# Performance work log

Measured on AMD Instinct MI355X. Metric: run time of the kernel, lower is better.

## Reference

```python
import jax, jax.numpy as jnp
import numpy as np

B, S, D = 1, 2048, 3072
H, DH = 24, 128
ENC, NIP = 512, 64
COND = (512 // 8) * (512 // 8) * 16 // 64  # 1024 cond tokens per lora
RANK, ALPHA, LW, IP_SCALE = 16, 16.0, 1.0, 1.0
EPS = 1e-5


def _rms(x):
    return x * jax.lax.rsqrt(jnp.mean(x * x, axis=-1, keepdims=True) + EPS)


def _to_heads(x):
    b, s, _ = x.shape
    return x.reshape(b, s, H, DH).transpose(0, 2, 1, 3)  # [B,H,S,DH]


def _from_heads(x):
    b, h, s, d = x.shape
    return x.transpose(0, 2, 1, 3).reshape(b, s, h * d)


def _lora(x, dn, up):
    # token mask keeps only the cond block (number=0, n_loras=1 -> last COND tokens)
    y = ((x[:, -COND:, :] @ dn) @ up) * (ALPHA / RANK)
    z = jnp.zeros((x.shape[0], x.shape[1] - COND, up.shape[1]), x.dtype)
    return jnp.concatenate([z, y], axis=1)


def _sdpa(q, k, v, mask=None):
    s = jnp.einsum('bhqd,bhkd->bhqk', q, k) * (1.0 / np.sqrt(DH))
    if mask is not None:
        s = s + mask
    return jnp.einsum('bhqk,bhkd->bhqd', jax.nn.softmax(s, axis=-1), v)


def _forward(hidden_states, encoder_hidden_states, image_emb,
             Wq, bq, Wk, bk, Wv, bv, Waq, baq, Wak, bak, Wav, bav,
             Wo, bo, Wao, bao, Wkip, Wvip,
             lq_dn, lq_up, lk_dn, lk_up, lv_dn, lv_up, lp_dn, lp_up):
    hs, ehs, img = hidden_states, encoder_hidden_states, image_emb
    # context (encoder) projections + RMSNorm on q/k
    eq = _rms(_to_heads(ehs @ Waq + baq))
    ek = _rms(_to_heads(ehs @ Wak + bak))
    ev = _to_heads(ehs @ Wav + bav)
    # main-stream q/k/v with masked LoRA branches
    q = hs @ Wq + bq + LW * _lora(hs, lq_dn, lq_up)
    k = hs @ Wk + bk + LW * _lora(hs, lk_dn, lk_up)
    v = hs @ Wv + bv + LW * _lora(hs, lv_dn, lv_up)
    q = _rms(_to_heads(q))
    k = _rms(_to_heads(k))
    v = _to_heads(v)
    # IP-adapter branch: extra K/V from image_emb, norm_added_k is RMSNorm(128)
    kip = _rms(_to_heads(img @ Wkip))
    vip = _to_heads(img @ Wvip)
    ip_out = _from_heads(_sdpa(q, kip, vip))  # [B,S,D]
    # concat encoder stream ahead of main stream
    q = jnp.concatenate([eq, q], axis=2)
    k = jnp.concatenate([ek, k], axis=2)
    v = jnp.concatenate([ev, v], axis=2)
    SL = ENC + S
    SB = SL - COND  # scaled_block_size
    m = jnp.ones((SL, SL), jnp.float32)
    m = m.at[:SB, :].set(0.0)        # non-cond rows attend everywhere
    m = m.at[SB:, SB:].set(0.0)      # single cond block attends to itself (n_loras=1)
    mask = m * (-1e20)
    out = _from_heads(_sdpa(q, k, v, mask))  # [B,SL,D]
    enc_out = out[:, :ENC, :]
    main = out[:, ENC:, :] + IP_SCALE * ip_out
    main = main @ Wo + bo
    main = main + LW * _lora(main, lp_dn, lp_up)  # proj LoRA (to_out dropout=identity)
    enc_out = enc_out @ Wao + bao
    return jnp.concatenate([enc_out, main], axis=1)  # [B, ENC+S, D]


def setup_inputs():
    key = jax.random.key(0)
    ks = iter(jax.random.split(key, 40))
    w = lambda *sh: jax.random.normal(next(ks), sh, jnp.float32) * 0.02
    return dict(
        hidden_states=jax.random.normal(next(ks), (B, S, D), jnp.float32),
        encoder_hidden_states=jax.random.normal(next(ks), (B, ENC, D), jnp.float32),
        image_emb=jax.random.normal(next(ks), (B, NIP, D), jnp.float32),
        Wq=w(D, D), bq=w(D), Wk=w(D, D), bk=w(D), Wv=w(D, D), bv=w(D),
        Waq=w(D, D), baq=w(D), Wak=w(D, D), bak=w(D), Wav=w(D, D), bav=w(D),
        Wo=w(D, D), bo=w(D), Wao=w(D, D), bao=w(D),
        Wkip=w(D, D), Wvip=w(D, D),
        lq_dn=w(D, RANK), lq_up=w(RANK, D), lk_dn=w(D, RANK), lk_up=w(RANK, D),
        lv_dn=w(D, RANK), lv_up=w(RANK, D), lp_dn=w(D, RANK), lp_up=w(RANK, D),
    )


def reference(hidden_states, encoder_hidden_states, image_emb,
              Wq, bq, Wk, bk, Wv, bv, Waq, baq, Wak, bak, Wav, bav,
              Wo, bo, Wao, bao, Wkip, Wvip,
              lq_dn, lq_up, lk_dn, lk_up, lv_dn, lv_up, lp_dn, lp_up):
    return _forward(hidden_states, encoder_hidden_states, image_emb,
                    Wq, bq, Wk, bk, Wv, bv, Waq, baq, Wak, bak, Wav, bav,
                    Wo, bo, Wao, bao, Wkip, Wvip,
                    lq_dn, lq_up, lk_dn, lk_up, lv_dn, lv_up, lp_dn, lp_up)
```

## Files before the change

kernel.cpp:

```cpp
#include <hip/hip_runtime.h>

typedef unsigned short u16;
typedef short s16x8 __attribute__((ext_vector_type(8)));
typedef float f32x4 __attribute__((ext_vector_type(4)));
typedef const __attribute__((address_space(1))) unsigned int* as1_u32p;
typedef __attribute__((address_space(3))) unsigned int* as3_u32p;

static_assert(sizeof(s16x8) == 16, "");

struct alignas(8) U16x4 { u16 x, y, z, w; };

__device__ __forceinline__ u16 f2bf(float f) {
  union { float f; unsigned u; } c; c.f = f;
  return (u16)((c.u + 0x7fffu + ((c.u >> 16) & 1u)) >> 16);
}
__device__ __forceinline__ float bf2f(u16 h) {
  union { unsigned u; float f; } c; c.u = ((unsigned)h) << 16;
  return c.f;
}
__device__ __forceinline__ void async16(const void* g, void* l) {
  __builtin_amdgcn_global_load_lds((as1_u32p)g, (as3_u32p)l, 16, 0, 0);
}

__launch_bounds__(256)
__global__ void cvt_bf16(const float* __restrict__ in, u16* __restrict__ out, long n) {
  long i = ((long)blockIdx.x * 256 + threadIdx.x) * 8;
  if (i >= n) return;
  float4 a = *(const float4*)(in + i);
  float4 b = *(const float4*)(in + i + 4);
  U16x4 o0{f2bf(a.x), f2bf(a.y), f2bf(a.z), f2bf(a.w)};
  U16x4 o1{f2bf(b.x), f2bf(b.y), f2bf(b.z), f2bf(b.w)};
  *(U16x4*)(out + i) = o0;
  *(U16x4*)(out + i + 4) = o1;
}

__launch_bounds__(256)
__global__ void cvt_hs(const float* __restrict__ hs, const float* __restrict__ tl,
                       u16* __restrict__ hsb) {
  long idx = (long)blockIdx.x * 256 + threadIdx.x;
  long m = idx / 392, c = idx % 392;
  U16x4 o0, o1;
  if (c < 384) {
    const float* p = hs + m * 3072 + c * 8;
    float4 a = *(const float4*)p;
    float4 b = *(const float4*)(p + 4);
    o0 = U16x4{f2bf(a.x), f2bf(a.y), f2bf(a.z), f2bf(a.w)};
    o1 = U16x4{f2bf(b.x), f2bf(b.y), f2bf(b.z), f2bf(b.w)};
  } else {
    u16 t[8];
#pragma unroll
    for (int i = 0; i < 8; ++i) {
      int r = (int)(c - 384) * 8 + i;
      float v = (m >= 1024 && r < 48) ? tl[(m - 1024) * 48 + r] : 0.f;
      t[i] = f2bf(v);
    }
    o0 = U16x4{t[0], t[1], t[2], t[3]};
    o1 = U16x4{t[4], t[5], t[6], t[7]};
  }
  u16* d = hsb + m * 3136 + c * 8;
  *(U16x4*)d = o0;
  *(U16x4*)(d + 4) = o1;
}

__launch_bounds__(256)
__global__ void pack_bias(const float* __restrict__ a, const float* __restrict__ b,
                          const float* __restrict__ c, float* __restrict__ out) {
  int i = blockIdx.x * 256 + threadIdx.x;
  if (i >= 9216) return;
  out[i] = (i < 3072) ? a[i] : (i < 6144) ? b[i - 3072] : c[i - 6144];
}

struct WTArgs { const float* src[3]; u16* dst[3]; };

__launch_bounds__(256)
__global__ void transpose_w(WTArgs args, int ldd) {
  const float* src = args.src[blockIdx.z];
  u16* dst = args.dst[blockIdx.z];
  __shared__ float tile[32][33];
  int k0 = blockIdx.x * 32, n0 = blockIdx.y * 32;
  int r = threadIdx.x >> 3, c4 = (threadIdx.x & 7) * 4;
  float4 v = *(const float4*)(src + (long)(k0 + r) * 3072 + n0 + c4);
  tile[r][c4 + 0] = v.x; tile[r][c4 + 1] = v.y;
  tile[r][c4 + 2] = v.z; tile[r][c4 + 3] = v.w;
  __syncthreads();
  U16x4 o{f2bf(tile[c4 + 0][r]), f2bf(tile[c4 + 1][r]),
          f2bf(tile[c4 + 2][r]), f2bf(tile[c4 + 3][r])};
  *(U16x4*)(dst + (long)(n0 + r) * ldd + k0 + c4) = o;
}

__launch_bounds__(256)
__global__ void fill_wtail(const float* __restrict__ u0, const float* __restrict__ u1,
                           const float* __restrict__ u2, u16* __restrict__ WTb) {
  int idx = blockIdx.x * 256 + threadIdx.x;
  int n = idx >> 6, i = idx & 63;
  int seg = n / 3072;
  const float* up = (seg == 0) ? u0 : (seg == 1) ? u1 : u2;
  int r = i - seg * 16;
  float v = (r >= 0 && r < 16) ? up[(long)r * 3072 + (n - seg * 3072)] : 0.f;
  WTb[(long)n * 3136 + 3072 + i] = f2bf(v);
}

__launch_bounds__(256)
__global__ void transpose_v(const u16* __restrict__ VB, u16* __restrict__ VT, int T) {
  __shared__ u16 tile[32][34];
  int h = blockIdx.z;
  int t0 = blockIdx.x * 32, d0 = blockIdx.y * 32;
  int r = threadIdx.x >> 3, c4 = (threadIdx.x & 7) * 4;
  U16x4 v = *(const U16x4*)(VB + ((long)h * T + t0 + r) * 128 + d0 + c4);
  tile[r][c4 + 0] = v.x; tile[r][c4 + 1] = v.y;
  tile[r][c4 + 2] = v.z; tile[r][c4 + 3] = v.w;
  __syncthreads();
  U16x4 o{tile[c4 + 0][r], tile[c4 + 1][r], tile[c4 + 2][r], tile[c4 + 3][r]};
  *(U16x4*)(VT + ((long)h * 128 + d0 + r) * T + t0 + c4) = o;
}

__launch_bounds__(256)
__global__ void rms_heads4(const float* __restrict__ in, int col0,
                           u16* __restrict__ out, int do_rms) {
  const int t = blockIdx.x;
  const int w = threadIdx.x >> 6, lane = threadIdx.x & 63;
  const long ps = 64LL * 6144;
#pragma unroll
  for (int hh = 0; hh < 6; ++hh) {
    int h = w * 6 + hh;
    const float* x = in + (long)t * 6144 + col0 + h * 128 + lane * 2;
    float a = x[0] + x[ps] + x[2 * ps] + x[3 * ps];
    float b = x[1] + x[1 + ps] + x[1 + 2 * ps] + x[1 + 3 * ps];
    float scale = 1.f;
    if (do_rms) {
      float ss = a * a + b * b;
#pragma unroll
      for (int st = 1; st < 64; st <<= 1) ss += __shfl_xor(ss, st, 64);
      scale = rsqrtf(ss * (1.f / 128.f) + 1e-5f);
    }
    unsigned pa = f2bf(a * scale), pb = f2bf(b * scale);
    *(unsigned*)(out + ((long)h * 64 + t) * 128 + lane * 2) = pa | (pb << 16);
  }
}

__launch_bounds__(256)
__global__ void lora_dn3(const float* __restrict__ X, int ldx,
                         const float* __restrict__ d0, const float* __restrict__ d1,
                         const float* __restrict__ d2, float* __restrict__ t) {
  __shared__ float red[4][48];
  const int m = blockIdx.x;
  const float* xr = X + (long)m * ldx;
  float p[48];
#pragma unroll
  for (int r = 0; r < 48; ++r) p[r] = 0.f;
  for (int k = threadIdx.x; k < 3072; k += 256) {
    float a = xr[k];
    const float* e0 = d0 + (long)k * 16;
    const float* e1 = d1 + (long)k * 16;
    const float* e2 = d2 + (long)k * 16;
#pragma unroll
    for (int r = 0; r < 16; ++r) {
      p[r]      += a * e0[r];
      p[16 + r] += a * e1[r];
      p[32 + r] += a * e2[r];
    }
  }
#pragma unroll
  for (int r = 0; r < 48; ++r)
#pragma unroll
    for (int st = 1; st < 64; st <<= 1) p[r] += __shfl_xor(p[r], st, 64);
  int lane = threadIdx.x & 63, w = threadIdx.x >> 6;
  if (lane == 0) {
#pragma unroll
    for (int r = 0; r < 48; ++r) red[w][r] = p[r];
  }
  __syncthreads();
  if (threadIdx.x < 48) {
    int r = threadIdx.x;
    t[(long)m * 48 + r] = red[0][r] + red[1][r] + red[2][r] + red[3][r];
  }
}

__launch_bounds__(256)
__global__ void lora_dn(const float* __restrict__ X, int ldx,
                        const float* __restrict__ dn, float* __restrict__ t) {
  __shared__ float red[4][16];
  const int m = blockIdx.x;
  const float* xr = X + (long)m * ldx;
  float p[16];
#pragma unroll
  for (int r = 0; r < 16; ++r) p[r] = 0.f;
  for (int k = threadIdx.x; k < 3072; k += 256) {
    float a = xr[k];
    const float* d = dn + (long)k * 16;
#pragma unroll
    for (int r = 0; r < 16; ++r) p[r] += a * d[r];
  }
#pragma unroll
  for (int r = 0; r < 16; ++r)
#pragma unroll
    for (int st = 1; st < 64; st <<= 1) p[r] += __shfl_xor(p[r], st, 64);
  int lane = threadIdx.x & 63, w = threadIdx.x >> 6;
  if (lane == 0) {
#pragma unroll
    for (int r = 0; r < 16; ++r) red[w][r] = p[r];
  }
  __syncthreads();
  if (threadIdx.x < 16) {
    int r = threadIdx.x;
    t[(long)m * 16 + r] = red[0][r] + red[1][r] + red[2][r] + red[3][r];
  }
}

__launch_bounds__(256)
__global__ void lora_up(const float* __restrict__ t, const float* __restrict__ up,
                        float* __restrict__ Y, int ldy) {
  const int m = blockIdx.x;
  float tv[16];
#pragma unroll
  for (int r = 0; r < 16; ++r) tv[r] = t[(long)m * 16 + r];
  float* yr = Y + (long)m * ldy;
  for (int n = threadIdx.x; n < 3072; n += 256) {
    float a = 0.f;
#pragma unroll
    for (int r = 0; r < 16; ++r) a += tv[r] * up[(long)r * 3072 + n];
    yr[n] += a;
  }
}

template <int BM, int MI, int NI>
__launch_bounds__(256)
__global__ void gemm_f32(const u16* __restrict__ A, int lda,
                         const u16* __restrict__ B, int ldb,
                         float* __restrict__ C, int ldc,
                         const float* __restrict__ bias, int KC, long cstride) {
  constexpr int WCOLS = 128 / (NI * 16);
  constexpr int ABYTES = BM * 128;
  __shared__ char smem[ABYTES + 128 * 128];
  char* As = smem;
  char* Bs = smem + ABYTES;
  const int tid = threadIdx.x;
  const int w = tid >> 6, lane = tid & 63;
  const int lr = lane & 15, lg = lane >> 4;
  const int wr = w / WCOLS, wc = w % WCOLS;
  const int nbx = gridDim.x;
  const int nwg = nbx * gridDim.y;
  const int flat = blockIdx.y * nbx + blockIdx.x;
  const int swz = (flat & 7) * (nwg >> 3) + (flat >> 3);
  const long m0 = (long)(swz % nbx) * BM;
  const long n0 = (long)(swz / nbx) * 128;
  const int k0 = blockIdx.z * KC;
  C += blockIdx.z * cstride;
  f32x4 acc[MI][NI] = {};
  constexpr int ACH = BM / 32;
  for (int kb = k0; kb < k0 + KC; kb += 64) {
    __syncthreads();
#pragma unroll
    for (int i = 0; i < ACH; ++i) {
      int x = (tid + 256 * i) * 16;
      int row = x >> 7;
      int sx = x ^ ((row & 7) << 4);
      async16((const char*)(A + (m0 + row) * lda + kb) + (sx & 127),
              As + ((w << 10) + (i << 12)));
    }
#pragma unroll
    for (int i = 0; i < 4; ++i) {
      int x = (tid + 256 * i) * 16;
      int row = x >> 7;
      int sx = x ^ ((row & 7) << 4);
      async16((const char*)(B + (n0 + row) * ldb + kb) + (sx & 127),
              Bs + ((w << 10) + (i << 12)));
    }
    __syncthreads();
#pragma unroll
    for (int kc = 0; kc < 2; ++kc) {
      s16x8 af[MI], bfr[NI];
#pragma unroll
      for (int mi = 0; mi < MI; ++mi) {
        int row = wr * (MI * 16) + mi * 16 + lr;
        int b = ((row << 7) + kc * 64 + lg * 16) ^ ((row & 7) << 4);
        af[mi] = *(const s16x8*)(As + b);
      }
#pragma unroll
      for (int ni = 0; ni < NI; ++ni) {
        int row = wc * (NI * 16) + ni * 16 + lr;
        int b = ((row << 7) + kc * 64 + lg * 16) ^ ((row & 7) << 4);
        bfr[ni] = *(const s16x8*)(Bs + b);
      }
#pragma unroll
      for (int mi = 0; mi < MI; ++mi)
#pragma unroll
        for (int ni = 0; ni < NI; ++ni)
          acc[mi][ni] = __builtin_amdgcn_mfma_f32_16x16x32_bf16(af[mi], bfr[ni], acc[mi][ni], 0, 0, 0);
    }
  }
#pragma unroll
  for (int mi = 0; mi < MI; ++mi) {
#pragma unroll
    for (int ni = 0; ni < NI; ++ni) {
      long col = n0 + wc * (NI * 16) + ni * 16 + lr;
      float bv = bias ? bias[col] : 0.f;
#pragma unroll
      for (int j = 0; j < 4; ++j) {
        long row = m0 + wr * (MI * 16) + mi * 16 + lg * 4 + j;
        C[row * ldc + col] = acc[mi][ni][j] + bv;
      }
    }
  }
}

__launch_bounds__(256, 2)
__global__ void gemm_qkv(const u16* __restrict__ A, int lda,
                         const u16* __restrict__ B, int ldb,
                         u16* __restrict__ Qo, u16* __restrict__ Ko, u16* __restrict__ VTo,
                         int t0, const float* __restrict__ bias, int K) {
  __shared__ char smem[49152];
  char* As = smem;
  char* Bs = smem + 16384;
  const int tid = threadIdx.x;
  const int w = tid >> 6, lane = tid & 63;
  const int lr = lane & 15, lg = lane >> 4;
  const int wr = w >> 1, wc = w & 1;
  const int nbx = gridDim.x;
  const int nwg = nbx * gridDim.y;
  const int flat = blockIdx.y * nbx + blockIdx.x;
  const int swz = (flat & 7) * (nwg >> 3) + (flat >> 3);
  const long m0 = (long)(swz % nbx) * 128;
  const long n0 = (long)(swz / nbx) * 256;
  f32x4 acc[4][8] = {};
  for (int kb = 0; kb < K; kb += 64) {
    __syncthreads();
#pragma unroll
    for (int i = 0; i < 4; ++i) {
      int x = (tid + 256 * i) * 16;
      int row = x >> 7;
      int sx = (x & 127) ^ ((row & 7) << 4);
      async16((const char*)(A + (m0 + row) * lda + kb) + sx, As + x);
    }
#pragma unroll
    for (int i = 0; i < 8; ++i) {
      int x = (tid + 256 * i) * 16;
      int row = x >> 7;
      int sx = (x & 127) ^ ((row & 7) << 4);
      async16((const char*)(B + (n0 + row) * ldb + kb) + sx, Bs + x);
    }
    __syncthreads();
#pragma unroll
    for (int kc = 0; kc < 2; ++kc) {
      s16x8 af[4], bfr[8];
#pragma unroll
      for (int mi = 0; mi < 4; ++mi) {
        int row = wr * 64 + mi * 16 + lr;
        af[mi] = *(const s16x8*)(As + (row << 7) + ((kc * 64 + lg * 16) ^ ((row & 7) << 4)));
      }
#pragma unroll
      for (int ni = 0; ni < 8; ++ni) {
        int row = wc * 128 + ni * 16 + lr;
        bfr[ni] = *(const s16x8*)(Bs + (row << 7) + ((kc * 64 + lg * 16) ^ ((row & 7) << 4)));
      }
#pragma unroll
      for (int mi = 0; mi < 4; ++mi)
#pragma unroll
        for (int ni = 0; ni < 8; ++ni)
          acc[mi][ni] = __builtin_amdgcn_mfma_f32_16x16x32_bf16(af[mi], bfr[ni], acc[mi][ni], 0, 0, 0);
    }
  }
  const int seg = (int)(n0 / 3072);
  const int head0 = (int)((n0 % 3072) >> 7);
#pragma unroll
  for (int ni = 0; ni < 8; ++ni) {
    float bv = bias[n0 + wc * 128 + ni * 16 + lr];
#pragma unroll
    for (int mi = 0; mi < 4; ++mi)
#pragma unroll
      for (int j = 0; j < 4; ++j) acc[mi][ni][j] += bv;
  }
  float scl[4][4];
  if (seg < 2) {
#pragma unroll
    for (int mi = 0; mi < 4; ++mi)
#pragma unroll
      for (int j = 0; j < 4; ++j) {
        float s = 0.f;
#pragma unroll
        for (int ni = 0; ni < 8; ++ni) s += acc[mi][ni][j] * acc[mi][ni][j];
#pragma unroll
        for (int st = 1; st < 16; st <<= 1) s += __shfl_xor(s, st, 16);
        scl[mi][j] = rsqrtf(s * (1.f / 128.f) + 1e-5f);
      }
  }
#pragma unroll
  for (int ph = 0; ph < 2; ++ph) {
    __syncthreads();
    if (wc == ph) {
      if (seg < 2) {
#pragma unroll
        for (int mi = 0; mi < 4; ++mi)
#pragma unroll
          for (int ni = 0; ni < 8; ++ni) {
            int d2 = (ni * 16 + lr) * 2;
#pragma unroll
            for (int j = 0; j < 4; ++j) {
              int tok = wr * 64 + mi * 16 + lg * 4 + j;
              *(u16*)(smem + tok * 256 + (d2 ^ ((tok & 7) << 4))) =
                  f2bf(acc[mi][ni][j] * scl[mi][j]);
            }
          }
      } else {
#pragma unroll
        for (int mi = 0; mi < 4; ++mi)
#pragma unroll
          for (int ni = 0; ni < 8; ++ni) {
            int d = ni * 16 + lr;
            int tok0b = (wr * 64 + mi * 16 + lg * 4) * 2;
            U16x4 o{f2bf(acc[mi][ni][0]), f2bf(acc[mi][ni][1]),
                    f2bf(acc[mi][ni][2]), f2bf(acc[mi][ni][3])};
            *(U16x4*)(smem + d * 256 + (tok0b ^ ((d & 7) << 4))) = o;
          }
      }
    }
    __syncthreads();
    const int headp = head0 + ph;
#pragma unroll
    for (int i = 0; i < 8; ++i) {
      int x = (tid + 256 * i) * 16;
      int row = x >> 8, col = x & 255;
      s16x8 vdat = *(const s16x8*)(smem + row * 256 + (col ^ ((row & 7) << 4)));
      if (seg < 2) {
        u16* g = (seg == 0 ? Qo : Ko) + ((long)headp * 2560 + t0 + m0 + row) * 128;
        *(s16x8*)((char*)g + col) = vdat;
      } else {
        u16* g = VTo + ((long)headp * 128 + row) * 2560 + t0 + m0;
        *(s16x8*)((char*)g + col) = vdat;
      }
    }
  }
}

__launch_bounds__(256)
__global__ void gemm_out(const u16* __restrict__ Atok, const u16* __restrict__ WT,
                         float* __restrict__ outp, const float* __restrict__ bao,
                         const float* __restrict__ bo) {
  __shared__ char smem[128 * 128 + 128 * 128];
  char* As = smem;
  char* Bs = smem + 128 * 128;
  const int tid = threadIdx.x;
  const int w = tid >> 6, lane = tid & 63;
  const int lr = lane & 15, lg = lane >> 4;
  const int wr = w >> 1, wc = w & 1;
  const int flat = blockIdx.y * 20 + blockIdx.x;
  const int swz = (flat & 7) * 60 + (flat >> 3);
  const int mx = swz % 20;
  const long n0 = (long)(swz / 20) * 128;
  const u16* A;
  const u16* B;
  const float* bias;
  float* C;
  long m0;
  if (mx < 4) { A = Atok; B = WT; bias = bao; C = outp; m0 = (long)mx * 128; }
  else { A = Atok + 512L * 3072; B = WT + 3072L * 3136; bias = bo; C = outp + 512L * 3072; m0 = (long)(mx - 4) * 128; }
  f32x4 acc[4][4] = {};
  for (int kb = 0; kb < 3072; kb += 64) {
    __syncthreads();
#pragma unroll
    for (int i = 0; i < 4; ++i) {
      int x = (tid + 256 * i) * 16;
      int row = x >> 7;
      int sx = x ^ ((row & 7) << 4);
      async16((const char*)(A + (m0 + row) * 3072 + kb) + (sx & 127),
              As + ((w << 10) + (i << 12)));
    }
#pragma unroll
    for (int i = 0; i < 4; ++i) {
      int x = (tid + 256 * i) * 16;
      int row = x >> 7;
      int sx = x ^ ((row & 7) << 4);
      async16((const char*)(B + (n0 + row) * 3136 + kb) + (sx & 127),
              Bs + ((w << 10) + (i << 12)));
    }
    __syncthreads();
#pragma unroll
    for (int kc = 0; kc < 2; ++kc) {
      s16x8 af[4], bfr[4];
#pragma unroll
      for (int mi = 0; mi < 4; ++mi) {
        int row = wr * 64 + mi * 16 + lr;
        int b = ((row << 7) + kc * 64 + lg * 16) ^ ((row & 7) << 4);
        af[mi] = *(const s16x8*)(As + b);
      }
#pragma unroll
      for (int ni = 0; ni < 4; ++ni) {
        int row = wc * 64 + ni * 16 + lr;
        int b = ((row << 7) + kc * 64 + lg * 16) ^ ((row & 7) << 4);
        bfr[ni] = *(const s16x8*)(Bs + b);
      }
#pragma unroll
      for (int mi = 0; mi < 4; ++mi)
#pragma unroll
        for (int ni = 0; ni < 4; ++ni)
          acc[mi][ni] = __builtin_amdgcn_mfma_f32_16x16x32_bf16(af[mi], bfr[ni], acc[mi][ni], 0, 0, 0);
    }
  }
#pragma unroll
  for (int mi = 0; mi < 4; ++mi) {
#pragma unroll
    for (int ni = 0; ni < 4; ++ni) {
      long col = n0 + wc * 64 + ni * 16 + lr;
      float bv = bias[col];
#pragma unroll
      for (int j = 0; j < 4; ++j) {
        long row = m0 + wr * 64 + mi * 16 + lg * 4 + j;
        C[row * 3072 + col] = acc[mi][ni][j] + bv;
      }
    }
  }
}

__launch_bounds__(512, 4)
__global__ void attn_fused(const u16* __restrict__ QB, const u16* __restrict__ KB,
                           const u16* __restrict__ VT, const u16* __restrict__ KipB,
                           const u16* __restrict__ VipT, u16* __restrict__ OutTok) {
  __shared__ char smem[81920];
  const int tid = threadIdx.x, w = tid >> 6, lane = tid & 63;
  const int lr = lane & 15, lg = lane >> 4;
  const int h = blockIdx.y;
  const int q0 = blockIdx.x * 128;
  const bool ip = (q0 >= 512);
  const u16* Qrow = QB + (long)(h * 2560 + q0 + w * 16 + lr) * 128;
  s16x8 qf[4];
#pragma unroll
  for (int dc = 0; dc < 4; ++dc) qf[dc] = *(const s16x8*)(Qrow + dc * 32 + lg * 8);
  f32x4 accO[8] = {};
  float l_r[4] = {0.f, 0.f, 0.f, 0.f};
  const int kv0 = (q0 >= 1536) ? 1536 : 0;
  const float sc = 0.08838834764831845f;

  auto stage_main = [&](int kv, int buf) {
#pragma unroll
    for (int i = 0; i < 2; ++i) {
      int x = (tid + 512 * i) * 16;
      int row = x >> 8;
      int sx = x ^ ((row & 7) << 4);
      async16((const char*)(KB + (long)(h * 2560 + kv + row) * 128) + (sx & 255),
              smem + buf * 16384 + ((i << 13) + (w << 10)));
    }
#pragma unroll
    for (int i = 0; i < 2; ++i) {
      int x = (tid + 512 * i) * 16;
      int row = x >> 7;
      int sx = x ^ ((row & 7) << 4);
      async16((const char*)(VT + (long)(h * 128 + row) * 2560 + kv) + (sx & 127),
              smem + 32768 + buf * 16384 + ((i << 13) + (w << 10)));
    }
  };
  auto stage_ip = [&](int buf) {
#pragma unroll
    for (int i = 0; i < 2; ++i) {
      int x = (tid + 512 * i) * 16;
      int row = x >> 8;
      int sx = x ^ ((row & 7) << 4);
// ... 43 lines not shown
#pragma unroll
    for (int kc = 0; kc < 2; ++kc) {
      int pb = ((lr << 7) + kc * 64 + lg * 16) ^ ((lr & 7) << 4);
      s16x8 pf = *(const s16x8*)(Pw + pb);
#pragma unroll
      for (int dt = 0; dt < 8; ++dt) {
        int row = dt * 16 + lr;
        int b = ((row << 7) + kc * 64 + lg * 16) ^ ((row & 7) << 4);
        s16x8 vf = *(const s16x8*)(Vs + b);
        accO[dt] = __builtin_amdgcn_mfma_f32_16x16x32_bf16(pf, vf, accO[dt], 0, 0, 0);
      }
    }
    __syncthreads();
    cur ^= 1;
  }
#pragma unroll
  for (int j = 0; j < 4; ++j) {
#pragma unroll
    for (int st = 1; st < 16; st <<= 1) l_r[j] += __shfl_xor(l_r[j], st, 16);
    l_r[j] = 1.f / l_r[j];
  }
#pragma unroll
  for (int dt = 0; dt < 8; ++dt)
#pragma unroll
    for (int j = 0; j < 4; ++j) accO[dt][j] *= l_r[j];
  if (ip) {
    const char* Ks = smem + cur * 16384;
    const char* Vs = smem + 32768 + cur * 16384;
    char* Pw = smem + 65536 + w * 2048;
    f32x4 s2[4] = {};
#pragma unroll
    for (int kt = 0; kt < 4; ++kt)
#pragma unroll
      for (int dc = 0; dc < 4; ++dc) {
        int row = kt * 16 + lr;
        int b = ((row << 8) + dc * 64 + lg * 16) ^ ((row & 7) << 4);
        s16x8 kf = *(const s16x8*)(Ks + b);
        s2[kt] = __builtin_amdgcn_mfma_f32_16x16x32_bf16(qf[dc], kf, s2[kt], 0, 0, 0);
      }
    float p2[4][4];
    float l2[4] = {0.f, 0.f, 0.f, 0.f};
#pragma unroll
    for (int kt = 0; kt < 4; ++kt)
#pragma unroll
      for (int j = 0; j < 4; ++j) {
        float pv = __expf(fmaf(s2[kt][j], sc, -12.0f));
        p2[kt][j] = pv;
        l2[j] += pv;
      }
#pragma unroll
    for (int j = 0; j < 4; ++j) {
#pragma unroll
      for (int st = 1; st < 16; st <<= 1) l2[j] += __shfl_xor(l2[j], st, 16);
      l2[j] = 1.f / l2[j];
    }
#pragma unroll
    for (int kt = 0; kt < 4; ++kt)
#pragma unroll
      for (int j = 0; j < 4; ++j) {
        int prow = lg * 4 + j;
        int b = ((prow << 7) + (kt * 16 + lr) * 2) ^ ((prow & 7) << 4);
        *(u16*)(Pw + b) = f2bf(p2[kt][j] * l2[j]);
      }
    asm volatile("s_waitcnt lgkmcnt(0)" ::: "memory");
#pragma unroll
    for (int kc = 0; kc < 2; ++kc) {
      int pb = ((lr << 7) + kc * 64 + lg * 16) ^ ((lr & 7) << 4);
      s16x8 pf = *(const s16x8*)(Pw + pb);
#pragma unroll
      for (int dt = 0; dt < 8; ++dt) {
        int row = dt * 16 + lr;
        int b = ((row << 7) + kc * 64 + lg * 16) ^ ((row & 7) << 4);
        s16x8 vf = *(const s16x8*)(Vs + b);
        accO[dt] = __builtin_amdgcn_mfma_f32_16x16x32_bf16(pf, vf, accO[dt], 0, 0, 0);
      }
    }
  }
#pragma unroll
  for (int j = 0; j < 4; ++j) {
    long tok = q0 + w * 16 + lg * 4 + j;
#pragma unroll
    for (int dt = 0; dt < 8; ++dt) {
      long col = h * 128 + dt * 16 + lr;
      OutTok[tok * 3072 + col] = f2bf(accO[dt][j]);
    }
  }
}


extern "C" void kernel_launch(void* const* d_in, const int* in_sizes, int n_in,
                              void* d_out, int out_size, void* d_ws, size_t ws_size,
                              hipStream_t stream) {
  const float* hs    = (const float*)d_in[0];
  const float* ehs   = (const float*)d_in[1];
  const float* img   = (const float*)d_in[2];
  const float* Wq    = (const float*)d_in[3];
  const float* bq    = (const float*)d_in[4];
  const float* Wk    = (const float*)d_in[5];
  const float* bk    = (const float*)d_in[6];
  const float* Wv    = (const float*)d_in[7];
  const float* bv    = (const float*)d_in[8];
  const float* Waq   = (const float*)d_in[9];
  const float* baq   = (const float*)d_in[10];
  const float* Wak   = (const float*)d_in[11];
  const float* bak   = (const float*)d_in[12];
  const float* Wav   = (const float*)d_in[13];
  const float* bav   = (const float*)d_in[14];
  const float* Wo    = (const float*)d_in[15];
  const float* bo    = (const float*)d_in[16];
  const float* Wao   = (const float*)d_in[17];
  const float* bao   = (const float*)d_in[18];
  const float* Wkip  = (const float*)d_in[19];
  const float* Wvip  = (const float*)d_in[20];
  const float* lq_dn = (const float*)d_in[21];
  const float* lq_up = (const float*)d_in[22];
  const float* lk_dn = (const float*)d_in[23];
  const float* lk_up = (const float*)d_in[24];
  const float* lv_dn = (const float*)d_in[25];
  const float* lv_up = (const float*)d_in[26];
  const float* lp_dn = (const float*)d_in[27];
  const float* lp_up = (const float*)d_in[28];
  float* outp = (float*)d_out;

  char* ws = (char*)d_ws;
  size_t off = 0;
  auto take = [&](size_t b) { char* p = ws + off; off += (b + 255) & ~(size_t)255; return p; };
  u16*   WTb  = (u16*)take(9216LL * 3136 * 2);
  u16*   hsb  = (u16*)take(2048LL * 3136 * 2);
  u16*   ehsb = (u16*)take(512LL * 3072 * 2);
  u16*   imgb = (u16*)take(64LL * 3072 * 2);
  u16*   QBf  = (u16*)take(24LL * 2560 * 128 * 2);
  u16*   KBf  = (u16*)take(24LL * 2560 * 128 * 2);
  u16*   VTf  = (u16*)take(24LL * 128 * 2560 * 2);
  u16*   AttnTok = (u16*)take(2560LL * 3072 * 2);
  float* IP0  = (float*)take(4LL * 64 * 6144 * 4);
  u16*   KipB = (u16*)take(24LL * 64 * 128 * 2);
  u16*   VipB = (u16*)take(24LL * 64 * 128 * 2);
  u16*   VipT = (u16*)take(24LL * 128 * 64 * 2);
  float* bpk  = (float*)take(9216 * 4);
  float* tl   = (float*)take(1024LL * 48 * 4);

  lora_dn3<<<1024, 256, 0, stream>>>(hs + 1024LL * 3072, 3072, lq_dn, lk_dn, lv_dn, tl);
  cvt_hs<<<3136, 256, 0, stream>>>(hs, tl, hsb);
  cvt_bf16<<<768, 256, 0, stream>>>(ehs, ehsb, 512LL * 3072);
  cvt_bf16<<<96, 256, 0, stream>>>(img, imgb, 64LL * 3072);

  pack_bias<<<36, 256, 0, stream>>>(baq, bak, bav, bpk);
  {
    WTArgs a;
    a.src[0] = Waq; a.dst[0] = WTb;
    a.src[1] = Wak; a.dst[1] = WTb + 3072LL * 3136;
    a.src[2] = Wav; a.dst[2] = WTb + 2 * 3072LL * 3136;
    transpose_w<<<dim3(96, 96, 3), 256, 0, stream>>>(a, 3136);
  }
  gemm_qkv<<<dim3(4, 36), 256, 0, stream>>>(ehsb, 3072, WTb, 3136, QBf, KBf, VTf, 0, bpk, 3072);

  {
    WTArgs a;
    a.src[0] = Wkip; a.dst[0] = WTb;
    a.src[1] = Wvip; a.dst[1] = WTb + 3072LL * 3136;
    a.src[2] = Wkip; a.dst[2] = WTb;
    transpose_w<<<dim3(96, 96, 2), 256, 0, stream>>>(a, 3136);
  }
  gemm_f32<64, 4, 2><<<dim3(1, 48, 4), 256, 0, stream>>>(imgb, 3072, WTb, 3136, IP0, 6144,
                                                          nullptr, 768, 64LL * 6144);
  rms_heads4<<<64, 256, 0, stream>>>(IP0, 0, KipB, 1);
  rms_heads4<<<64, 256, 0, stream>>>(IP0, 3072, VipB, 0);
  transpose_v<<<dim3(2, 4, 24), 256, 0, stream>>>(VipB, VipT, 64);

  pack_bias<<<36, 256, 0, stream>>>(bq, bk, bv, bpk);
  {
    WTArgs a;
    a.src[0] = Wq; a.dst[0] = WTb;
    a.src[1] = Wk; a.dst[1] = WTb + 3072LL * 3136;
    a.src[2] = Wv; a.dst[2] = WTb + 2 * 3072LL * 3136;
    transpose_w<<<dim3(96, 96, 3), 256, 0, stream>>>(a, 3136);
  }
  fill_wtail<<<2304, 256, 0, stream>>>(lq_up, lk_up, lv_up, WTb);
  gemm_qkv<<<dim3(16, 36), 256, 0, stream>>>(hsb, 3136, WTb, 3136, QBf, KBf, VTf, 512, bpk, 3136);

  attn_fused<<<dim3(20, 24), 512, 0, stream>>>(QBf, KBf, VTf, KipB, VipT, AttnTok);

  {
    WTArgs a;
    a.src[0] = Wao; a.dst[0] = WTb;
    a.src[1] = Wo;  a.dst[1] = WTb + 3072LL * 3136;
    a.src[2] = Wao; a.dst[2] = WTb;
    transpose_w<<<dim3(96, 96, 2), 256, 0, stream>>>(a, 3136);
  }
  gemm_out<<<dim3(20, 24), 256, 0, stream>>>(AttnTok, WTb, outp, bao, bo);

  lora_dn<<<1024, 256, 0, stream>>>(outp + 1536LL * 3072, 3072, lp_dn, tl);
  lora_up<<<1024, 256, 0, stream>>>(tl, lp_up, outp + 1536LL * 3072, 3072);
}
```

Baseline: 668.5 us.

## Merge encoder/main QKV GEMMs, fold output LoRA into out-proj GEMM, batch prep kernels

Merges the encoder and main-stream QKV projections into one gemm_qkv launch over a 20x36 grid, and combines all fp32-to-bf16 conversion, bias packing and LoRA-tail filling into a single prep_all kernel. The output-projection LoRA is folded algebraically: Wo·lp_dn and bo·lp_dn are precomputed (Wod), the rank-16 down-projection of the attention output is written into a K-tail of the attention token buffer, and lp_up is appended to the transposed Wo, so gemm_out absorbs the LoRA. Weight transposes are batched into fewer launches, Q/K are staged in the output buffer and hsb is reused for the attention output to save workspace. The goal is fewer launches, better GPU fill on the QKV GEMM and no separate read-modify-write LoRA pass on the output. The cost is an extra 3073-row reduction kernel, a slightly longer K for the main out-projection, and some precision change from bf16-rounding the LoRA tail.

```diff
diff --git a/kernel.cpp b/kernel.cpp
--- a/kernel.cpp
+++ b/kernel.cpp
@@ -23,59 +23,148 @@
 }
 
 __launch_bounds__(256)
-__global__ void cvt_bf16(const float* __restrict__ in, u16* __restrict__ out, long n) {
-  long i = ((long)blockIdx.x * 256 + threadIdx.x) * 8;
-  if (i >= n) return;
-  float4 a = *(const float4*)(in + i);
-  float4 b = *(const float4*)(in + i + 4);
-  U16x4 o0{f2bf(a.x), f2bf(a.y), f2bf(a.z), f2bf(a.w)};
-  U16x4 o1{f2bf(b.x), f2bf(b.y), f2bf(b.z), f2bf(b.w)};
-  *(U16x4*)(out + i) = o0;
-  *(U16x4*)(out + i + 4) = o1;
-}
-
-__launch_bounds__(256)
-__global__ void cvt_hs(const float* __restrict__ hs, const float* __restrict__ tl,
-                       u16* __restrict__ hsb) {
-  long idx = (long)blockIdx.x * 256 + threadIdx.x;
-  long m = idx / 392, c = idx % 392;
-  U16x4 o0, o1;
-  if (c < 384) {
-    const float* p = hs + m * 3072 + c * 8;
-    float4 a = *(const float4*)p;
-    float4 b = *(const float4*)(p + 4);
-    o0 = U16x4{f2bf(a.x), f2bf(a.y), f2bf(a.z), f2bf(a.w)};
-    o1 = U16x4{f2bf(b.x), f2bf(b.y), f2bf(b.z), f2bf(b.w)};
+__global__ void lora_dn3(const float* __restrict__ X, int ldx,
+                         const float* __restrict__ d0, const float* __restrict__ d1,
+                         const float* __restrict__ d2, float* __restrict__ t) {
+  __shared__ float red[4][48];
+  const int m = blockIdx.x;
+  const float* xr = X + (long)m * ldx;
+  float p[48];
+#pragma unroll
+  for (int r = 0; r < 48; ++r) p[r] = 0.f;
+  for (int k = threadIdx.x; k < 3072; k += 256) {
+    float a = xr[k];
+    const float* e0 = d0 + (long)k * 16;
+    const float* e1 = d1 + (long)k * 16;
+    const float* e2 = d2 + (long)k * 16;
+#pragma unroll
+    for (int r = 0; r < 16; ++r) {
+      p[r]      += a * e0[r];
+      p[16 + r] += a * e1[r];
+      p[32 + r] += a * e2[r];
+    }
+  }
+#pragma unroll
+  for (int r = 0; r < 48; ++r)
+#pragma unroll
+    for (int st = 1; st < 64; st <<= 1) p[r] += __shfl_xor(p[r], st, 64);
+  int lane = threadIdx.x & 63, w = threadIdx.x >> 6;
+  if (lane == 0) {
+#pragma unroll
+    for (int r = 0; r < 48; ++r) red[w][r] = p[r];
+  }
+  __syncthreads();
+  if (threadIdx.x < 48) {
+    int r = threadIdx.x;
+    t[(long)m * 48 + r] = red[0][r] + red[1][r] + red[2][r] + red[3][r];
+  }
+}
+
+__launch_bounds__(256)
+__global__ void wod_prep(const float* __restrict__ Wo, const float* __restrict__ bo,
+                         const float* __restrict__ dn, float* __restrict__ Wod) {
+  __shared__ float red[4][16];
+  const int m = blockIdx.x;
+  const float* xr = (m < 3072) ? Wo + (long)m * 3072 : bo;
+  float p[16];
+#pragma unroll
+  for (int r = 0; r < 16; ++r) p[r] = 0.f;
+  for (int k = threadIdx.x; k < 3072; k += 256) {
+    float a = xr[k];
+    const float* d = dn + (long)k * 16;
+#pragma unroll
+    for (int r = 0; r < 16; ++r) p[r] += a * d[r];
+  }
+#pragma unroll
+  for (int r = 0; r < 16; ++r)
+#pragma unroll
+    for (int st = 1; st < 64; st <<= 1) p[r] += __shfl_xor(p[r], st, 64);
+  int lane = threadIdx.x & 63, w = threadIdx.x >> 6;
+  if (lane == 0) {
+#pragma unroll
+    for (int r = 0; r < 16; ++r) red[w][r] = p[r];
+  }
+  __syncthreads();
+  if (threadIdx.x < 16) {
+    int r = threadIdx.x;
+    Wod[(long)m * 16 + r] = red[0][r] + red[1][r] + red[2][r] + red[3][r];
+  }
+}
+
+__launch_bounds__(256)
+__global__ void prep_all(const float* __restrict__ hs, const float* __restrict__ tl,
+                         u16* __restrict__ hsb,
+                         const float* __restrict__ ehs, u16* __restrict__ ehsb,
+                         const float* __restrict__ img, u16* __restrict__ imgb,
+                         const float* __restrict__ baq, const float* __restrict__ bak,
+                         const float* __restrict__ bav, const float* __restrict__ bq,
+                         const float* __restrict__ bk, const float* __restrict__ bv,
+                         float* __restrict__ bpk,
+                         const float* __restrict__ u0, const float* __restrict__ u1,
+                         const float* __restrict__ u2, u16* __restrict__ WTbM) {
+  const int b = blockIdx.x;
+  if (b < 3136) {
+    long idx = (long)b * 256 + threadIdx.x;
+    long m = idx / 392, c = idx % 392;
+    U16x4 o0, o1;
+    if (c < 384) {
+      const float* p = hs + m * 3072 + c * 8;
+      float4 a = *(const float4*)p;
+      float4 bb = *(const float4*)(p + 4);
+      o0 = U16x4{f2bf(a.x), f2bf(a.y), f2bf(a.z), f2bf(a.w)};
+      o1 = U16x4{f2bf(bb.x), f2bf(bb.y), f2bf(bb.z), f2bf(bb.w)};
+    } else {
+      u16 t[8];
+#pragma unroll
+      for (int i = 0; i < 8; ++i) {
+        int r = (int)(c - 384) * 8 + i;
+        float v = (m >= 1024 && r < 48) ? tl[(m - 1024) * 48 + r] : 0.f;
+        t[i] = f2bf(v);
+      }
+      o0 = U16x4{t[0], t[1], t[2], t[3]};
+      o1 = U16x4{t[4], t[5], t[6], t[7]};
+    }
+    u16* d = hsb + m * 3136 + c * 8;
+    *(U16x4*)d = o0;
+    *(U16x4*)(d + 4) = o1;
+  } else if (b < 3904) {
+    long i = ((long)(b - 3136) * 256 + threadIdx.x) * 8;
+    float4 a = *(const float4*)(ehs + i);
+    float4 bb = *(const float4*)(ehs + i + 4);
+    *(U16x4*)(ehsb + i) = U16x4{f2bf(a.x), f2bf(a.y), f2bf(a.z), f2bf(a.w)};
+    *(U16x4*)(ehsb + i + 4) = U16x4{f2bf(bb.x), f2bf(bb.y), f2bf(bb.z), f2bf(bb.w)};
+  } else if (b < 4000) {
+    long i = ((long)(b - 3904) * 256 + threadIdx.x) * 8;
+    float4 a = *(const float4*)(img + i);
+    float4 bb = *(const float4*)(img + i + 4);
+    *(U16x4*)(imgb + i) = U16x4{f2bf(a.x), f2bf(a.y), f2bf(a.z), f2bf(a.w)};
+    *(U16x4*)(imgb + i + 4) = U16x4{f2bf(bb.x), f2bf(bb.y), f2bf(bb.z), f2bf(bb.w)};
+  } else if (b < 4072) {
+    int i = (b - 4000) * 256 + threadIdx.x;
+    if (i < 9216)
+      bpk[i] = (i < 3072) ? baq[i] : (i < 6144) ? bak[i - 3072] : bav[i - 6144];
+    else {
+      int j = i - 9216;
+      bpk[i] = (j < 3072) ? bq[j] : (j < 6144) ? bk[j - 3072] : bv[j - 6144];
+    }
   } else {
-    u16 t[8];
-#pragma unroll
-    for (int i = 0; i < 8; ++i) {
-      int r = (int)(c - 384) * 8 + i;
-      float v = (m >= 1024 && r < 48) ? tl[(m - 1024) * 48 + r] : 0.f;
-      t[i] = f2bf(v);
-    }
-    o0 = U16x4{t[0], t[1], t[2], t[3]};
-    o1 = U16x4{t[4], t[5], t[6], t[7]};
-  }
-  u16* d = hsb + m * 3136 + c * 8;
-  *(U16x4*)d = o0;
-  *(U16x4*)(d + 4) = o1;
-}
-
-__launch_bounds__(256)
-__global__ void pack_bias(const float* __restrict__ a, const float* __restrict__ b,
-                          const float* __restrict__ c, float* __restrict__ out) {
-  int i = blockIdx.x * 256 + threadIdx.x;
-  if (i >= 9216) return;
-  out[i] = (i < 3072) ? a[i] : (i < 6144) ? b[i - 3072] : c[i - 6144];
-}
-
-struct WTArgs { const float* src[3]; u16* dst[3]; };
-
-__launch_bounds__(256)
-__global__ void transpose_w(WTArgs args, int ldd) {
+    int idx = (b - 4072) * 256 + threadIdx.x;
+    int n = idx >> 6, i = idx & 63;
+    int seg = n / 3072;
+    const float* up = (seg == 0) ? u0 : (seg == 1) ? u1 : u2;
+    int r = i - seg * 16;
+    float v = (r >= 0 && r < 16) ? up[(long)r * 3072 + (n - seg * 3072)] : 0.f;
+    WTbM[(long)n * 3136 + 3072 + i] = f2bf(v);
+  }
+}
+
+struct WT6 { const float* src[6]; u16* dst[6]; int ldd[6]; };
+
+__launch_bounds__(256)
+__global__ void transpose_w(WT6 args) {
   const float* src = args.src[blockIdx.z];
   u16* dst = args.dst[blockIdx.z];
+  const int ldd = args.ldd[blockIdx.z];
   __shared__ float tile[32][33];
   int k0 = blockIdx.x * 32, n0 = blockIdx.y * 32;
   int r = threadIdx.x >> 3, c4 = (threadIdx.x & 7) * 4;
@@ -89,137 +178,50 @@
 }
 
 __launch_bounds__(256)
-__global__ void fill_wtail(const float* __restrict__ u0, const float* __restrict__ u1,
-                           const float* __restrict__ u2, u16* __restrict__ WTb) {
+__global__ void fill_wo_tail(const float* __restrict__ lp_up, u16* __restrict__ WTbM) {
   int idx = blockIdx.x * 256 + threadIdx.x;
   int n = idx >> 6, i = idx & 63;
-  int seg = n / 3072;
-  const float* up = (seg == 0) ? u0 : (seg == 1) ? u1 : u2;
-  int r = i - seg * 16;
-  float v = (r >= 0 && r < 16) ? up[(long)r * 3072 + (n - seg * 3072)] : 0.f;
-  WTb[(long)n * 3136 + 3072 + i] = f2bf(v);
-}
-
-__launch_bounds__(256)
-__global__ void transpose_v(const u16* __restrict__ VB, u16* __restrict__ VT, int T) {
-  __shared__ u16 tile[32][34];
-  int h = blockIdx.z;
-  int t0 = blockIdx.x * 32, d0 = blockIdx.y * 32;
-  int r = threadIdx.x >> 3, c4 = (threadIdx.x & 7) * 4;
-  U16x4 v = *(const U16x4*)(VB + ((long)h * T + t0 + r) * 128 + d0 + c4);
-  tile[r][c4 + 0] = v.x; tile[r][c4 + 1] = v.y;
-  tile[r][c4 + 2] = v.z; tile[r][c4 + 3] = v.w;
-  __syncthreads();
-  U16x4 o{tile[c4 + 0][r], tile[c4 + 1][r], tile[c4 + 2][r], tile[c4 + 3][r]};
-  *(U16x4*)(VT + ((long)h * 128 + d0 + r) * T + t0 + c4) = o;
-}
-
-__launch_bounds__(256)
-__global__ void rms_heads4(const float* __restrict__ in, int col0,
-                           u16* __restrict__ out, int do_rms) {
-  const int t = blockIdx.x;
-  const int w = threadIdx.x >> 6, lane = threadIdx.x & 63;
-  const long ps = 64LL * 6144;
-#pragma unroll
-  for (int hh = 0; hh < 6; ++hh) {
-    int h = w * 6 + hh;
-    const float* x = in + (long)t * 6144 + col0 + h * 128 + lane * 2;
-    float a = x[0] + x[ps] + x[2 * ps] + x[3 * ps];
-    float b = x[1] + x[1 + ps] + x[1 + 2 * ps] + x[1 + 3 * ps];
-    float scale = 1.f;
-    if (do_rms) {
-      float ss = a * a + b * b;
-#pragma unroll
-      for (int st = 1; st < 64; st <<= 1) ss += __shfl_xor(ss, st, 64);
-      scale = rsqrtf(ss * (1.f / 128.f) + 1e-5f);
-    }
-    unsigned pa = f2bf(a * scale), pb = f2bf(b * scale);
-    *(unsigned*)(out + ((long)h * 64 + t) * 128 + lane * 2) = pa | (pb << 16);
-  }
-}
-
-__launch_bounds__(256)
-__global__ void lora_dn3(const float* __restrict__ X, int ldx,
-                         const float* __restrict__ d0, const float* __restrict__ d1,
-                         const float* __restrict__ d2, float* __restrict__ t) {
-  __shared__ float red[4][48];
-  const int m = blockIdx.x;
-  const float* xr = X + (long)m * ldx;
-  float p[48];
-#pragma unroll
-  for (int r = 0; r < 48; ++r) p[r] = 0.f;
-  for (int k = threadIdx.x; k < 3072; k += 256) {
-    float a = xr[k];
-    const float* e0 = d0 + (long)k * 16;
-    const float* e1 = d1 + (long)k * 16;
-    const float* e2 = d2 + (long)k * 16;
-#pragma unroll
-    for (int r = 0; r < 16; ++r) {
-      p[r]      += a * e0[r];
-      p[16 + r] += a * e1[r];
-      p[32 + r] += a * e2[r];
-    }
-  }
-#pragma unroll
-  for (int r = 0; r < 48; ++r)
+  float v = (i < 16) ? lp_up[(long)i * 3072 + n] : 0.f;
+  WTbM[(long)n * 3136 + 3072 + i] = f2bf(v);
+}
+
+__launch_bounds__(256)
+__global__ void t_tail(u16* __restrict__ At, const float* __restrict__ Wod) {
+  __shared__ float red[4][16];
+  const int tok = blockIdx.x;
+  u16* tail = At + (long)(512 + tok) * 3136 + 3072;
+  if (tok < 1024) {
+    if (threadIdx.x < 64) tail[threadIdx.x] = 0;
+    return;
+  }
+  const u16* xr = At + (long)(512 + tok) * 3136;
+  float p[16];
+#pragma unroll
+  for (int r = 0; r < 16; ++r) p[r] = 0.f;
+  for (int n = threadIdx.x; n < 3072; n += 256) {
+    float a = bf2f(xr[n]);
+    const float* wd = Wod + (long)n * 16;
+#pragma unroll
+    for (int r = 0; r < 16; ++r) p[r] += a * wd[r];
+  }
+#pragma unroll
+  for (int r = 0; r < 16; ++r)
 #pragma unroll
     for (int st = 1; st < 64; st <<= 1) p[r] += __shfl_xor(p[r], st, 64);
   int lane = threadIdx.x & 63, w = threadIdx.x >> 6;
   if (lane == 0) {
 #pragma unroll
-    for (int r = 0; r < 48; ++r) red[w][r] = p[r];
+    for (int r = 0; r < 16; ++r) red[w][r] = p[r];
   }
   __syncthreads();
-  if (threadIdx.x < 48) {
-    int r = threadIdx.x;
-    t[(long)m * 48 + r] = red[0][r] + red[1][r] + red[2][r] + red[3][r];
-  }
-}
-
-__launch_bounds__(256)
-__global__ void lora_dn(const float* __restrict__ X, int ldx,
-                        const float* __restrict__ dn, float* __restrict__ t) {
-  __shared__ float red[4][16];
-  const int m = blockIdx.x;
-  const float* xr = X + (long)m * ldx;
-  float p[16];
-#pragma unroll
-  for (int r = 0; r < 16; ++r) p[r] = 0.f;
-  for (int k = threadIdx.x; k < 3072; k += 256) {
-    float a = xr[k];
-    const float* d = dn + (long)k * 16;
-#pragma unroll
-    for (int r = 0; r < 16; ++r) p[r] += a * d[r];
-  }
-#pragma unroll
-  for (int r = 0; r < 16; ++r)
-#pragma unroll
-    for (int st = 1; st < 64; st <<= 1) p[r] += __shfl_xor(p[r], st, 64);
-  int lane = threadIdx.x & 63, w = threadIdx.x >> 6;
-  if (lane == 0) {
-#pragma unroll
-    for (int r = 0; r < 16; ++r) red[w][r] = p[r];
-  }
-  __syncthreads();
-  if (threadIdx.x < 16) {
-    int r = threadIdx.x;
-    t[(long)m * 16 + r] = red[0][r] + red[1][r] + red[2][r] + red[3][r];
-  }
-}
-
-__launch_bounds__(256)
-__global__ void lora_up(const float* __restrict__ t, const float* __restrict__ up,
-                        float* __restrict__ Y, int ldy) {
-  const int m = blockIdx.x;
-  float tv[16];
-#pragma unroll
-  for (int r = 0; r < 16; ++r) tv[r] = t[(long)m * 16 + r];
-  float* yr = Y + (long)m * ldy;
-  for (int n = threadIdx.x; n < 3072; n += 256) {
-    float a = 0.f;
-#pragma unroll
-    for (int r = 0; r < 16; ++r) a += tv[r] * up[(long)r * 3072 + n];
-    yr[n] += a;
+  if (threadIdx.x < 64) {
+    if (threadIdx.x < 16) {
+      int r = threadIdx.x;
+      float t = red[0][r] + red[1][r] + red[2][r] + red[3][r] + Wod[3072L * 16 + r];
+      tail[r] = f2bf(t);
+    } else {
+      tail[threadIdx.x] = 0;
+    }
   }
 }
 
@@ -304,11 +306,52 @@
   }
 }
 
+__launch_bounds__(256)
+__global__ void rms_ip(const float* __restrict__ in, u16* __restrict__ Ko,
+                       u16* __restrict__ Vo) {
+  const int t = blockIdx.x & 63;
+  const int vhalf = blockIdx.x >> 6;
+  const int col0 = vhalf ? 3072 : 0;
+  u16* out = vhalf ? Vo : Ko;
+  const int w = threadIdx.x >> 6, lane = threadIdx.x & 63;
+  const long ps = 64LL * 6144;
+#pragma unroll
+  for (int hh = 0; hh < 6; ++hh) {
+    int h = w * 6 + hh;
+    const float* x = in + (long)t * 6144 + col0 + h * 128 + lane * 2;
+    float a = x[0] + x[ps] + x[2 * ps] + x[3 * ps];
+    float b = x[1] + x[1 + ps] + x[1 + 2 * ps] + x[1 + 3 * ps];
+    float scale = 1.f;
+    if (!vhalf) {
+      float ss = a * a + b * b;
+#pragma unroll
+      for (int st = 1; st < 64; st <<= 1) ss += __shfl_xor(ss, st, 64);
+      scale = rsqrtf(ss * (1.f / 128.f) + 1e-5f);
+    }
+    unsigned pa = f2bf(a * scale), pb = f2bf(b * scale);
+    *(unsigned*)(out + ((long)h * 64 + t) * 128 + lane * 2) = pa | (pb << 16);
+  }
+}
+
+__launch_bounds__(256)
+__global__ void transpose_v(const u16* __restrict__ VB, u16* __restrict__ VT, int T) {
+  __shared__ u16 tile[32][34];
+  int h = blockIdx.z;
+  int t0 = blockIdx.x * 32, d0 = blockIdx.y * 32;
+  int r = threadIdx.x >> 3, c4 = (threadIdx.x & 7) * 4;
+  U16x4 v = *(const U16x4*)(VB + ((long)h * T + t0 + r) * 128 + d0 + c4);
+  tile[r][c4 + 0] = v.x; tile[r][c4 + 1] = v.y;
+  tile[r][c4 + 2] = v.z; tile[r][c4 + 3] = v.w;
+  __syncthreads();
+  U16x4 o{tile[c4 + 0][r], tile[c4 + 1][r], tile[c4 + 2][r], tile[c4 + 3][r]};
+  *(U16x4*)(VT + ((long)h * 128 + d0 + r) * T + t0 + c4) = o;
+}
+
 __launch_bounds__(256, 2)
-__global__ void gemm_qkv(const u16* __restrict__ A, int lda,
-                         const u16* __restrict__ B, int ldb,
+__global__ void gemm_qkv(const u16* __restrict__ Aenc, const u16* __restrict__ Amain,
+                         const u16* __restrict__ Benc, const u16* __restrict__ Bmain,
                          u16* __restrict__ Qo, u16* __restrict__ Ko, u16* __restrict__ VTo,
-                         int t0, const float* __restrict__ bias, int K) {
+                         const float* __restrict__ bpk) {
   __shared__ char smem[49152];
   char* As = smem;
   char* Bs = smem + 16384;
@@ -316,12 +359,22 @@
   const int w = tid >> 6, lane = tid & 63;
   const int lr = lane & 15, lg = lane >> 4;
   const int wr = w >> 1, wc = w & 1;
-  const int nbx = gridDim.x;
-  const int nwg = nbx * gridDim.y;
-  const int flat = blockIdx.y * nbx + blockIdx.x;
-  const int swz = (flat & 7) * (nwg >> 3) + (flat >> 3);
-  const long m0 = (long)(swz % nbx) * 128;
-  const long n0 = (long)(swz / nbx) * 256;
+  const int flat = blockIdx.y * 20 + blockIdx.x;
+  const int swz = (flat & 7) * 90 + (flat >> 3);
+  const int mx = swz % 20;
+  const long n0 = (long)(swz / 20) * 256;
+  const u16* A;
+  const u16* B;
+  const float* bias;
+  int lda, ldb, K, t0;
+  long m0;
+  if (mx < 4) {
+    A = Aenc; lda = 3072; B = Benc; ldb = 3072; K = 3072; t0 = 0;
+    m0 = (long)mx * 128; bias = bpk;
+  } else {
+    A = Amain; lda = 3136; B = Bmain; ldb = 3136; K = 3136; t0 = 512;
+    m0 = (long)(mx - 4) * 128; bias = bpk + 9216;
+  }
   f32x4 acc[4][8] = {};
   for (int kb = 0; kb < K; kb += 64) {
     __syncthreads();
@@ -433,9 +486,9 @@
 }
 
 __launch_bounds__(256)
-__global__ void gemm_out(const u16* __restrict__ Atok, const u16* __restrict__ WT,
-                         float* __restrict__ outp, const float* __restrict__ bao,
-                         const float* __restrict__ bo) {
+__global__ void gemm_out(const u16* __restrict__ Atok, const u16* __restrict__ Benc,
+                         const u16* __restrict__ Bmain, float* __restrict__ outp,
+                         const float* __restrict__ bao, const float* __restrict__ bo) {
   __shared__ char smem[128 * 128 + 128 * 128];
   char* As = smem;
   char* Bs = smem + 128 * 128;
@@ -451,18 +504,24 @@
   const u16* B;
   const float* bias;
   float* C;
+  int ldb, K;
   long m0;
-  if (mx < 4) { A = Atok; B = WT; bias = bao; C = outp; m0 = (long)mx * 128; }
-  else { A = Atok + 512L * 3072; B = WT + 3072L * 3136; bias = bo; C = outp + 512L * 3072; m0 = (long)(mx - 4) * 128; }
+  if (mx < 4) {
+    A = Atok; B = Benc; ldb = 3072; K = 3072; bias = bao; C = outp;
+    m0 = (long)mx * 128;
+  } else {
+    A = Atok + 512L * 3136; B = Bmain; ldb = 3136; K = 3136; bias = bo;
+    C = outp + 512L * 3072; m0 = (long)(mx - 4) * 128;
+  }
   f32x4 acc[4][4] = {};
-  for (int kb = 0; kb < 3072; kb += 64) {
+  for (int kb = 0; kb < K; kb += 64) {
     __syncthreads();
 #pragma unroll
     for (int i = 0; i < 4; ++i) {
       int x = (tid + 256 * i) * 16;
       int row = x >> 7;
       int sx = x ^ ((row & 7) << 4);
-      async16((const char*)(A + (m0 + row) * 3072 + kb) + (sx & 127),
+      async16((const char*)(A + (m0 + row) * 3136 + kb) + (sx & 127),
               As + ((w << 10) + (i << 12)));
     }
 #pragma unroll
@@ -470,7 +529,7 @@
       int x = (tid + 256 * i) * 16;
       int row = x >> 7;
       int sx = x ^ ((row & 7) << 4);
-      async16((const char*)(B + (n0 + row) * 3136 + kb) + (sx & 127),
+      async16((const char*)(B + (n0 + row) * ldb + kb) + (sx & 127),
               Bs + ((w << 10) + (i << 12)));
     }
     __syncthreads();
@@ -680,7 +739,7 @@
 #pragma unroll
     for (int dt = 0; dt < 8; ++dt) {
       long col = h * 128 + dt * 16 + lr;
-      OutTok[tok * 3072 + col] = f2bf(accO[dt][j]);
+      OutTok[tok * 3136 + col] = f2bf(accO[dt][j]);
     }
   }
 }
@@ -723,71 +782,62 @@
   char* ws = (char*)d_ws;
   size_t off = 0;
   auto take = [&](size_t b) { char* p = ws + off; off += (b + 255) & ~(size_t)255; return p; };
-  u16*   WTb  = (u16*)take(9216LL * 3136 * 2);
+  u16*   WTbE = (u16*)take(3LL * 3072 * 3072 * 2);
+  u16*   WTbM = (u16*)take(3LL * 3072 * 3136 * 2);
   u16*   hsb  = (u16*)take(2048LL * 3136 * 2);
   u16*   ehsb = (u16*)take(512LL * 3072 * 2);
   u16*   imgb = (u16*)take(64LL * 3072 * 2);
-  u16*   QBf  = (u16*)take(24LL * 2560 * 128 * 2);
-  u16*   KBf  = (u16*)take(24LL * 2560 * 128 * 2);
   u16*   VTf  = (u16*)take(24LL * 128 * 2560 * 2);
-  u16*   AttnTok = (u16*)take(2560LL * 3072 * 2);
   float* IP0  = (float*)take(4LL * 64 * 6144 * 4);
   u16*   KipB = (u16*)take(24LL * 64 * 128 * 2);
   u16*   VipB = (u16*)take(24LL * 64 * 128 * 2);
   u16*   VipT = (u16*)take(24LL * 128 * 64 * 2);
-  float* bpk  = (float*)take(9216 * 4);
+  float* bpk  = (float*)take(2 * 9216 * 4);
   float* tl   = (float*)take(1024LL * 48 * 4);
+  float* Wod  = (float*)take(3073LL * 16 * 4);
+  u16* QBf = (u16*)d_out;
+  u16* KBf = (u16*)d_out + 24LL * 2560 * 128;
+  u16* AttnTok = hsb;
+  u16* E1 = WTbE + 3072LL * 3072;
 
   lora_dn3<<<1024, 256, 0, stream>>>(hs + 1024LL * 3072, 3072, lq_dn, lk_dn, lv_dn, tl);
-  cvt_hs<<<3136, 256, 0, stream>>>(hs, tl, hsb);
-  cvt_bf16<<<768, 256, 0, stream>>>(ehs, ehsb, 512LL * 3072);
-  cvt_bf16<<<96, 256, 0, stream>>>(img, imgb, 64LL * 3072);
-
-  pack_bias<<<36, 256, 0, stream>>>(baq, bak, bav, bpk);
+  prep_all<<<6376, 256, 0, stream>>>(hs, tl, hsb, ehs, ehsb, img, imgb,
+                                     baq, bak, bav, bq, bk, bv, bpk,
+                                     lq_up, lk_up, lv_up, WTbM);
+  wod_prep<<<3073, 256, 0, stream>>>(Wo, bo, lp_dn, Wod);
+
   {
-    WTArgs a;
-    a.src[0] = Waq; a.dst[0] = WTb;
-    a.src[1] = Wak; a.dst[1] = WTb + 3072LL * 3136;
-    a.src[2] = Wav; a.dst[2] = WTb + 2 * 3072LL * 3136;
-    transpose_w<<<dim3(96, 96, 3), 256, 0, stream>>>(a, 3136);
-  }
-  gemm_qkv<<<dim3(4, 36), 256, 0, stream>>>(ehsb, 3072, WTb, 3136, QBf, KBf, VTf, 0, bpk, 3072);
+    WT6 a;
+    a.src[0] = Waq; a.dst[0] = WTbE;                    a.ldd[0] = 3072;
+    a.src[1] = Wak; a.dst[1] = WTbE + 3072LL * 3072;    a.ldd[1] = 3072;
+    a.src[2] = Wav; a.dst[2] = WTbE + 2 * 3072LL * 3072; a.ldd[2] = 3072;
+    a.src[3] = Wq;  a.dst[3] = WTbM;                    a.ldd[3] = 3136;
+    a.src[4] = Wk;  a.dst[4] = WTbM + 3072LL * 3136;    a.ldd[4] = 3136;
+    a.src[5] = Wv;  a.dst[5] = WTbM + 2 * 3072LL * 3136; a.ldd[5] = 3136;
+    transpose_w<<<dim3(96, 96, 6), 256, 0, stream>>>(a);
+  }
+
+  gemm_qkv<<<dim3(20, 36), 256, 0, stream>>>(ehsb, hsb, WTbE, WTbM, QBf, KBf, VTf, bpk);
 
   {
-    WTArgs a;
-    a.src[0] = Wkip; a.dst[0] = WTb;
-    a.src[1] = Wvip; a.dst[1] = WTb + 3072LL * 3136;
-    a.src[2] = Wkip; a.dst[2] = WTb;
-    transpose_w<<<dim3(96, 96, 2), 256, 0, stream>>>(a, 3136);
-  }
-  gemm_f32<64, 4, 2><<<dim3(1, 48, 4), 256, 0, stream>>>(imgb, 3072, WTb, 3136, IP0, 6144,
+    WT6 a;
+    a.src[0] = Wao;  a.dst[0] = WTbE;                    a.ldd[0] = 3072;
+    a.src[1] = Wkip; a.dst[1] = E1;                      a.ldd[1] = 3072;
+    a.src[2] = Wvip; a.dst[2] = WTbE + 2 * 3072LL * 3072; a.ldd[2] = 3072;
+    a.src[3] = Wo;   a.dst[3] = WTbM;                    a.ldd[3] = 3136;
+    a.src[4] = Wao;  a.dst[4] = WTbE;                    a.ldd[4] = 3072;
+    a.src[5] = Wao;  a.dst[5] = WTbE;                    a.ldd[5] = 3072;
+    transpose_w<<<dim3(96, 96, 4), 256, 0, stream>>>(a);
+  }
+  fill_wo_tail<<<768, 256, 0, stream>>>(lp_up, WTbM);
+
+  gemm_f32<64, 4, 2><<<dim3(1, 48, 4), 256, 0, stream>>>(imgb, 3072, E1, 3072, IP0, 6144,
                                                           nullptr, 768, 64LL * 6144);
-  rms_heads4<<<64, 256, 0, stream>>>(IP0, 0, KipB, 1);
-  rms_heads4<<<64, 256, 0, stream>>>(IP0, 3072, VipB, 0);
+  rms_ip<<<128, 256, 0, stream>>>(IP0, KipB, VipB);
   transpose_v<<<dim3(2, 4, 24), 256, 0, stream>>>(VipB, VipT, 64);
 
-  pack_bias<<<36, 256, 0, stream>>>(bq, bk, bv, bpk);
-  {
-    WTArgs a;
-    a.src[0] = Wq; a.dst[0] = WTb;
-    a.src[1] = Wk; a.dst[1] = WTb + 3072LL * 3136;
-    a.src[2] = Wv; a.dst[2] = WTb + 2 * 3072LL * 3136;
-    transpose_w<<<dim3(96, 96, 3), 256, 0, stream>>>(a, 3136);
-  }
-  fill_wtail<<<2304, 256, 0, stream>>>(lq_up, lk_up, lv_up, WTb);
-  gemm_qkv<<<dim3(16, 36), 256, 0, stream>>>(hsb, 3136, WTb, 3136, QBf, KBf, VTf, 512, bpk, 3136);
-
   attn_fused<<<dim3(20, 24), 512, 0, stream>>>(QBf, KBf, VTf, KipB, VipT, AttnTok);
 
-  {
-    WTArgs a;
-    a.src[0] = Wao; a.dst[0] = WTb;
-    a.src[1] = Wo;  a.dst[1] = WTb + 3072LL * 3136;
-    a.src[2] = Wao; a.dst[2] = WTb;
-    transpose_w<<<dim3(96, 96, 2), 256, 0, stream>>>(a, 3136);
-  }
-  gemm_out<<<dim3(20, 24), 256, 0, stream>>>(AttnTok, WTb, outp, bao, bo);
-
-  lora_dn<<<1024, 256, 0, stream>>>(outp + 1536LL * 3072, 3072, lp_dn, tl);
-  lora_up<<<1024, 256, 0, stream>>>(tl, lp_up, outp + 1536LL * 3072, 3072);
-}
+  t_tail<<<2048, 256, 0, stream>>>(AttnTok, Wod);
+  gemm_out<<<dim3(20, 24), 256, 0, stream>>>(AttnTok, WTbE, WTbM, outp, bao, bo);
+}
```

Measured after the change: 642.5 us. -3.9%, faster.
